# Optimization experiments

Hardware: AMD Instinct MI355X
Metric: run time of the kernel (lower is better)

Reference implementation:

```python
import jax, jax.numpy as jnp
import numpy as np

EPS_BN = 1e-5
EPS_NORM = 1e-12


def setup_inputs() -> dict:
    dim, mid, k = 128, 32, 3
    b, h, w = 8, 128, 128
    key = jax.random.key(0)
    ks = jax.random.split(key, 16)
    s = 0.05
    return {
        "x": jax.random.normal(ks[0], (b, dim, h, w), jnp.float32),
        "w_spatial_in": jax.random.normal(ks[1], (dim, dim), jnp.float32) * s,
        "w_dw_spatial": jax.random.normal(ks[2], (dim, 1, k), jnp.float32) * s,
        "w_spatial_out": jax.random.normal(ks[3], (dim, dim), jnp.float32) * s,
        "w_ch_in": jax.random.normal(ks[4], (dim, dim), jnp.float32) * s,
        "w_ch_dw": jax.random.normal(ks[5], (dim, 1, k), jnp.float32) * s,
        "w_ch_out": jax.random.normal(ks[6], (dim, dim), jnp.float32) * s,
        "w_mlp1": jax.random.normal(ks[7], (mid, dim), jnp.float32) * s,
        "b_mlp1": jax.random.normal(ks[8], (mid,), jnp.float32) * s,
        "w_mlp2": jax.random.normal(ks[9], (dim, mid), jnp.float32) * s,
        "b_mlp2": jax.random.normal(ks[10], (dim,), jnp.float32) * s,
        "diff_weight": jnp.float32(1.0),
        "bn_gamma": jnp.ones((dim,), jnp.float32),
        "bn_beta": jnp.zeros((dim,), jnp.float32),
        "w_out_proj": jax.random.normal(ks[11], (dim, dim), jnp.float32) * s,
    }


def _dwconv1d(seq, wk):
    # seq: [b, c, L], wk: [c, 1, k] depthwise, 'same' padding
    c = seq.shape[1]
    k = wk.shape[-1]
    return jax.lax.conv_general_dilated(
        seq, wk, window_strides=(1,), padding=[(k // 2, k // 2)],
        dimension_numbers=("NCH", "OIH", "NCH"), feature_group_count=c)


def _ocs_forward(x, w_spatial_in, w_dw_spatial, w_spatial_out,
                 w_ch_in, w_ch_dw, w_ch_out,
                 w_mlp1, b_mlp1, w_mlp2, b_mlp2,
                 diff_weight, bn_gamma, bn_beta, w_out_proj):
    b, c, h, w = x.shape
    L = h * w
    alpha = beta = eta = 1.0

    # ---- scan indices (4 orders) ----
    idx_row = jnp.arange(L)
    gy, gx = jnp.meshgrid(jnp.arange(h), jnp.arange(w), indexing="ij")
    idx_col = (gx * h + gy).reshape(-1)
    orders = [idx_row, idx_row[::-1], idx_col, idx_col[::-1]]

    x_seq0 = x.reshape(b, c, L).transpose(0, 2, 1)  # [b, L, c]

    def scan(idx):
        s = x_seq0[:, idx]                                   # gather   [b,L,c]
        s = jnp.einsum("blc,oc->blo", s, w_spatial_in)       # linear
        s = _dwconv1d(s.transpose(0, 2, 1), w_dw_spatial)    # dw conv  [b,c,L]
        s = jnp.einsum("bcl,oc->blo", s, w_spatial_out)      # linear   [b,L,c]
        s = s.at[:, idx].set(s[:, jnp.arange(L)]) if False else s[:, jnp.argsort(idx)]  # scatter back (inverse perm)
        return s.transpose(0, 2, 1).reshape(b, c, h, w)

    y_sp = (scan(orders[0]) + scan(orders[1]) + scan(orders[2]) + scan(orders[3])) * 0.25

    # ---- channel branch ----
    seq = x.reshape(b, c, L)
    seq = jnp.einsum("oc,bcl->bol", w_ch_in, seq)
    seq = _dwconv1d(seq, w_ch_dw)
    seq = jnp.einsum("oc,bcl->bol", w_ch_out, seq)
    gap = x.mean((2, 3))                                     # [b,c]
    gap = gap / jnp.maximum(jnp.linalg.norm(gap, axis=1, keepdims=True), EPS_NORM)
    m = jnp.einsum("bi,bj->bij", gap, gap)                   # [b,c,c]
    seq_agg = jnp.einsum("bij,bjl->bil", m, seq)             # [b,c,L]
    h1 = jax.nn.silu(jnp.einsum("mc,bcl->bml", w_mlp1, seq_agg) + b_mlp1[None, :, None])
    y_ch = (jnp.einsum("cm,bml->bcl", w_mlp2, h1) + b_mlp2[None, :, None]).reshape(b, c, h, w)

    # ---- difference branch (reflect-pad 4-neighbor abs diff) ----
    p = jnp.pad(x, ((0, 0), (0, 0), (1, 1), (1, 1)), mode="reflect")
    cx = p[:, :, 1:-1, 1:-1]
    diff = (jnp.abs(cx - p[:, :, 1:-1, :-2]) + jnp.abs(cx - p[:, :, 1:-1, 2:])
            + jnp.abs(cx - p[:, :, :-2, 1:-1]) + jnp.abs(cx - p[:, :, 2:, 1:-1])) * 0.25
    y_diff = x + diff_weight * diff

    # ---- combine, 1x1 proj, batchnorm (training-mode batch stats) ----
    y = alpha * y_sp + beta * y_ch + eta * y_diff
    y = jnp.einsum("oc,bchw->bohw", w_out_proj, y)
    mu = y.mean((0, 2, 3))
    var = y.var((0, 2, 3))
    y = (y - mu[None, :, None, None]) * jax.lax.rsqrt(var + EPS_BN)[None, :, None, None]
    y = y * bn_gamma[None, :, None, None] + bn_beta[None, :, None, None]
    return y


def reference(x, w_spatial_in, w_dw_spatial, w_spatial_out, w_ch_in, w_ch_dw,
              w_ch_out, w_mlp1, b_mlp1, w_mlp2, b_mlp2, diff_weight,
              bn_gamma, bn_beta, w_out_proj):
    return _ocs_forward(x, w_spatial_in, w_dw_spatial, w_spatial_out,
                        w_ch_in, w_ch_dw, w_ch_out, w_mlp1, b_mlp1,
                        w_mlp2, b_mlp2, diff_weight, bn_gamma, bn_beta,
                        w_out_proj)
```

## Files before the change

### kernel.cpp

```cpp
#include <hip/hip_runtime.h>
#include <hip/hip_bf16.h>

#define C 128
#define L 16384
#define B 8
#define MID 32
#define NBL (B * L)

typedef unsigned short ushort_t;
typedef __attribute__((ext_vector_type(8))) short s8v;
typedef __attribute__((ext_vector_type(4))) float f4v;
typedef __attribute__((ext_vector_type(8))) float f8v;

__device__ __forceinline__ unsigned short f2bf(float f) {
    union { float f; unsigned int u; } a; a.f = f;
    unsigned int u = a.u;
    return (unsigned short)((u + 0x7fffu + ((u >> 16) & 1u)) >> 16);
}

__device__ __forceinline__ f8v unp8(s8v v) {
    f8v f;
#pragma unroll
    for (int j = 0; j < 8; j++) f[j] = __uint_as_float(((unsigned int)(unsigned short)v[j]) << 16);
    return f;
}

__device__ __forceinline__ f8v ldf8(const float* p) {
    float4 a = *(const float4*)p;
    float4 b = *(const float4*)(p + 4);
    f8v f;
    f[0] = a.x; f[1] = a.y; f[2] = a.z; f[3] = a.w;
    f[4] = b.x; f[5] = b.y; f[6] = b.z; f[7] = b.w;
    return f;
}

__device__ __forceinline__ int widx(int slot, int o, int w) {
    return ((slot * 8 + (o >> 4)) * 64 + (w >> 3) * 16 + (o & 15)) * 8 + (w & 7);
}

__global__ __launch_bounds__(256) void k_cvt(const float* __restrict__ x,
                                             ushort_t* __restrict__ xb,
                                             float* __restrict__ gap) {
    __shared__ float xs[64][129];
    const int bid = blockIdx.x;
    const int b = bid >> 8;
    const int l0 = (bid & 255) * 64;
    const int tid = threadIdx.x;
    const int c = tid >> 1, h = tid & 1;
    const float* src = x + ((size_t)(b * C + c)) * L + l0 + h * 32;
    float s = 0.f;
#pragma unroll
    for (int j = 0; j < 8; j++) {
        float4 v = *(const float4*)(src + j * 4);
        s += (v.x + v.y) + (v.z + v.w);
        int lb = h * 32 + j * 4;
        xs[lb + 0][c] = v.x; xs[lb + 1][c] = v.y;
        xs[lb + 2][c] = v.z; xs[lb + 3][c] = v.w;
    }
    s += __shfl_xor(s, 1);
    if (h == 0) atomicAdd(&gap[b * C + c], s);
    __syncthreads();
    const int l = tid & 63, quarter = tid >> 6, cb = quarter * 32;
    union { ushort_t hh[32]; uint4 q[4]; } u;
#pragma unroll
    for (int k = 0; k < 32; k++) u.hh[k] = f2bf(xs[l][cb + k]);
    uint4* dst = (uint4*)(xb + ((size_t)(b * L + l0 + l)) * C + cb);
#pragma unroll
    for (int k = 0; k < 4; k++) dst[k] = u.q[k];
}

__global__ __launch_bounds__(128) void k_prep(const float* __restrict__ Win,
                                              const float* __restrict__ Wproj,
                                              const float* __restrict__ Wout,
                                              const float* __restrict__ w2,
                                              const float* __restrict__ b2,
                                              const float* __restrict__ wds,
                                              const float* __restrict__ gap,
                                              const float* __restrict__ w1,
                                              const float* __restrict__ Wco,
                                              const float* __restrict__ wcd,
                                              const float* __restrict__ Wci,
                                              ushort_t* __restrict__ Wf,
                                              float* __restrict__ bp,
                                              float* __restrict__ a,
                                              float* __restrict__ pv) {
    const int bid = blockIdx.x;
    const int c = threadIdx.x;
    if (bid < 128) {
        const int o = bid;
        __shared__ float pr[C];
        __shared__ float wct[C];
        pr[c] = Wproj[o * C + c];
        __syncthreads();
        {
            float s = 0.f;
            for (int k = 0; k < C; k++) s = fmaf(pr[k], Wout[k * C + c], s);
            wct[c] = s;
        }
        __syncthreads();
        float a1 = 0.f, as = 0.f;
        for (int cc = 0; cc < C; cc++) {
            float w = wct[cc];
            float win = Win[cc * C + c];
            a1 = fmaf(w * wds[3 * cc + 1], win, a1);
            as = fmaf(w * (0.25f * (wds[3 * cc] + wds[3 * cc + 2])), win, as);
        }
        const int slot = c >> 5, wi = c & 31;
        Wf[widx(slot, o, wi)] = f2bf(a1);
        Wf[widx(4 + slot, o, wi)] = f2bf(as);
        Wf[widx(8 + slot, o, wi)] = f2bf(pr[c]);
        if (c < MID) {
            float s2 = 0.f;
            for (int k = 0; k < C; k++) s2 = fmaf(pr[k], w2[k * MID + c], s2);
            Wf[widx(12, o, c)] = f2bf(s2);
        }
        if (c == 0) {
            float s3 = 0.f;
            for (int k = 0; k < C; k++) s3 = fmaf(pr[k], b2[k], s3);
            bp[o] = s3;
        }
    } else {
        const int b = bid - 128;
        __shared__ float gl[C];
        __shared__ float red[C];
        __shared__ float gws[C];
        float v = gap[b * C + c] * (1.f / (float)L);
        red[c] = v * v;
        __syncthreads();
        for (int w = 64; w > 0; w >>= 1) {
            if (c < w) red[c] += red[c + w];
            __syncthreads();
        }
        float nrm = fmaxf(sqrtf(red[0]), 1e-12f);
        gl[c] = v / nrm;
        __syncthreads();
        if (c < MID) {
            float s = 0.f;
            for (int k = 0; k < C; k++) s = fmaf(w1[c * C + k], gl[k], s);
            a[b * MID + c] = s;
        }
        {
            float s = 0.f;
            for (int k = 0; k < C; k++) s = fmaf(gl[k], Wco[k * C + c], s);
            gws[c] = s;
        }
        __syncthreads();
        float p0 = 0.f, p1 = 0.f, p2 = 0.f;
        for (int cc = 0; cc < C; cc++) {
            float wv = Wci[cc * C + c];
            float g = gws[cc];
            p0 = fmaf(g * wcd[3 * cc], wv, p0);
            p1 = fmaf(g * wcd[3 * cc + 1], wv, p1);
            p2 = fmaf(g * wcd[3 * cc + 2], wv, p2);
        }
        pv[b * 384 + c] = p0;
        pv[b * 384 + 128 + c] = p1;
        pv[b * 384 + 256 + c] = p2;
    }
}

__global__ __launch_bounds__(1024) __attribute__((amdgpu_waves_per_eu(4, 4)))
void k_fused(const ushort_t* __restrict__ xb,
             const ushort_t* __restrict__ Wf,
             const float* __restrict__ pv,
             const float* __restrict__ a,
             const float* __restrict__ b1,
             const float* __restrict__ pdw,
             const float* __restrict__ bp,
             float* __restrict__ outp,
             float* __restrict__ stats) {
    __shared__ ushort_t wlf[53248];
    __shared__ float spv[384];
    __shared__ float sdst[C];
    __shared__ float sdsq[C];
    const int tid = threadIdx.x;
    const int bid = blockIdx.x;
    const int b = bid & 7;
    const int rg = bid >> 3;

#pragma unroll
    for (int i = 0; i < 7; i++) {
        int idx = tid + i * 1024;
        if (idx < 6656) ((uint4*)wlf)[idx] = ((const uint4*)Wf)[idx];
    }
    if (tid < 384) spv[tid] = pv[b * 384 + tid];
    if (tid < C) { sdst[tid] = 0.f; sdsq[tid] = 0.f; }

    const int wave = tid >> 6, lane = tid & 63;
    const int n = lane & 15, q = lane >> 4;
    const int xg = (wave & 7) * 16 + n;
    const float dwt4 = pdw[0] * 0.25f;
    const size_t rb = (size_t)b * L;

    __syncthreads();

#define AF(slot, mt) (*(const s8v*)(wlf + ((((slot) * 8 + (mt)) * 64 + lane) * 8)))

#pragma unroll 1
    for (int iter = 0; iter < 2; iter++) {
        const int y = rg * 4 + iter * 2 + (wave >> 3);
        const int l = y * 128 + xg;

        const int rL = (l > 0) ? (l - 1) : -1;
        const int rR = (l < L - 1) ? (l + 1) : -1;
        const int rU = (y > 0) ? (l - 128) : ((xg > 0) ? (16256 + xg - 1) : -1);
        const int rD = (y < 127) ? (l + 128) : ((xg < 127) ? (xg + 1) : -1);
        const ushort_t* xrow = xb + (rb + l) * C;
        const ushort_t* prL = xb + (rb + ((rL >= 0) ? rL : 0)) * C;
        const ushort_t* prR = xb + (rb + ((rR >= 0) ? rR : 0)) * C;
        const ushort_t* prU = xb + (rb + ((rU >= 0) ? rU : 0)) * C;
        const ushort_t* prD = xb + (rb + ((rD >= 0) ? rD : 0)) * C;

        float s1 = 0.f;
#pragma unroll
        for (int ks = 0; ks < 4; ks++) {
            const int c0 = ks * 32 + q * 8;
            {
                f8v xv = unp8(*(const s8v*)(xrow + c0));
                f8v p = ldf8(spv + 128 + c0);
#pragma unroll
                for (int j = 0; j < 8; j++) s1 = fmaf(p[j], xv[j], s1);
            }
            {
                f8v xv = unp8(*(const s8v*)(prL + c0));
                if (rL < 0) {
#pragma unroll
                    for (int j = 0; j < 8; j++) xv[j] = 0.f;
                }
                f8v p = ldf8(spv + c0);
#pragma unroll
                for (int j = 0; j < 8; j++) s1 = fmaf(p[j], xv[j], s1);
            }
            {
                f8v xv = unp8(*(const s8v*)(prR + c0));
                if (rR < 0) {
#pragma unroll
                    for (int j = 0; j < 8; j++) xv[j] = 0.f;
                }
                f8v p = ldf8(spv + 256 + c0);
#pragma unroll
                for (int j = 0; j < 8; j++) s1 = fmaf(p[j], xv[j], s1);
            }
        }
        s1 += __shfl_xor(s1, 16);
        s1 += __shfl_xor(s1, 32);

        f4v acc[8];
#pragma unroll
        for (int i = 0; i < 8; i++) acc[i] = (f4v){0.f, 0.f, 0.f, 0.f};

        {
            f8v av = ldf8(a + b * MID + q * 8);
            f8v bv = ldf8(b1 + q * 8);
            s8v fs;
#pragma unroll
            for (int j = 0; j < 8; j++) {
                float pre = fmaf(av[j], s1, bv[j]);
                fs[j] = (short)f2bf(pre / (1.f + __expf(-pre)));
            }
#pragma unroll
            for (int mt = 0; mt < 8; mt++)
                acc[mt] = __builtin_amdgcn_mfma_f32_16x16x32_bf16(AF(12, mt), fs, acc[mt], 0, 0, 0);
        }

#pragma unroll
        for (int ks = 0; ks < 4; ks++) {
            const int c0 = ks * 32 + q * 8;
            s8v vc = *(const s8v*)(xrow + c0);
            s8v vl = *(const s8v*)(prL + c0);
            s8v vr = *(const s8v*)(prR + c0);
            s8v vu = *(const s8v*)(prU + c0);
            s8v vd = *(const s8v*)(prD + c0);
            if (rL < 0) vl = (s8v){0, 0, 0, 0, 0, 0, 0, 0};
            if (rR < 0) vr = (s8v){0, 0, 0, 0, 0, 0, 0, 0};
            if (rU < 0) vu = (s8v){0, 0, 0, 0, 0, 0, 0, 0};
            if (rD < 0) vd = (s8v){0, 0, 0, 0, 0, 0, 0, 0};

#pragma unroll
            for (int mt = 0; mt < 8; mt++)
                acc[mt] = __builtin_amdgcn_mfma_f32_16x16x32_bf16(AF(ks, mt), vc, acc[mt], 0, 0, 0);
#pragma unroll
            for (int mt = 0; mt < 8; mt++) {
                s8v af = AF(4 + ks, mt);
                acc[mt] = __builtin_amdgcn_mfma_f32_16x16x32_bf16(af, vl, acc[mt], 0, 0, 0);
                acc[mt] = __builtin_amdgcn_mfma_f32_16x16x32_bf16(af, vr, acc[mt], 0, 0, 0);
                acc[mt] = __builtin_amdgcn_mfma_f32_16x16x32_bf16(af, vu, acc[mt], 0, 0, 0);
                acc[mt] = __builtin_amdgcn_mfma_f32_16x16x32_bf16(af, vd, acc[mt], 0, 0, 0);
            }

            f8v xc = unp8(vc);
            f8v d8;
            {
                f8v t = unp8((xg > 0) ? vl : vr);
#pragma unroll
                for (int j = 0; j < 8; j++) d8[j] = fabsf(xc[j] - t[j]);
            }
            {
                f8v t = unp8((xg < 127) ? vr : vl);
#pragma unroll
                for (int j = 0; j < 8; j++) d8[j] += fabsf(xc[j] - t[j]);
            }
            {
                f8v t = unp8((y > 0) ? vu : vd);
#pragma unroll
                for (int j = 0; j < 8; j++) d8[j] += fabsf(xc[j] - t[j]);
            }
            {
                f8v t = unp8((y < 127) ? vd : vu);
#pragma unroll
                for (int j = 0; j < 8; j++) d8[j] += fabsf(xc[j] - t[j]);
            }
            s8v vy;
#pragma unroll
            for (int j = 0; j < 8; j++) vy[j] = (short)f2bf(fmaf(dwt4, d8[j], xc[j]));
#pragma unroll
            for (int mt = 0; mt < 8; mt++)
                acc[mt] = __builtin_amdgcn_mfma_f32_16x16x32_bf16(AF(8 + ks, mt), vy, acc[mt], 0, 0, 0);
        }

#pragma unroll
        for (int mt = 0; mt < 8; mt++) {
            const int o0 = mt * 16 + q * 4;
            float4 bv4 = *(const float4*)(bp + o0);
#pragma unroll
            for (int i = 0; i < 4; i++) {
                float bai = (i == 0) ? bv4.x : (i == 1) ? bv4.y : (i == 2) ? bv4.z : bv4.w;
                float v = acc[mt][i] + bai;
                outp[((size_t)(b * C + o0 + i)) * L + l] = v;
                float s = v, sq = v * v;
                s += __shfl_xor(s, 1); sq += __shfl_xor(sq, 1);
                s += __shfl_xor(s, 2); sq += __shfl_xor(sq, 2);
                s += __shfl_xor(s, 4); sq += __shfl_xor(sq, 4);
                s += __shfl_xor(s, 8); sq += __shfl_xor(sq, 8);
                if (n == 0) {
                    atomicAdd(&sdst[o0 + i], s);
                    atomicAdd(&sdsq[o0 + i], sq);
                }
            }
        }
    }

#undef AF

    __syncthreads();
    if (tid < C) {
        atomicAdd(&stats[tid], sdst[tid]);
        atomicAdd(&stats[C + tid], sdsq[tid]);
    }
}

__global__ __launch_bounds__(256) void k_bnapply(float* __restrict__ outp,
                                                 const float* __restrict__ stats,
                                                 const float* __restrict__ gamma,
                                                 const float* __restrict__ beta) {
    int bo = blockIdx.x;
    int o = bo & (C - 1);
    float nn = (float)NBL;
    float mu = stats[o] / nn;
    float var = stats[C + o] / nn - mu * mu;
    float sc = gamma[o] * rsqrtf(var + 1e-5f);
    float sh = fmaf(-mu, sc, beta[o]);
    float4* p = (float4*)(outp + (size_t)bo * L);
    for (int i = threadIdx.x; i < L / 4; i += 256) {
        float4 v = p[i];
        v.x = fmaf(v.x, sc, sh);
        v.y = fmaf(v.y, sc, sh);
        v.z = fmaf(v.z, sc, sh);
        v.w = fmaf(v.w, sc, sh);
        p[i] = v;
    }
}

extern "C" void kernel_launch(void* const* d_in, const int* in_sizes, int n_in,
                              void* d_out, int out_size, void* d_ws, size_t ws_size,
                              hipStream_t stream) {
    const float* x = (const float*)d_in[0];
    const float* Win = (const float*)d_in[1];
    const float* wds = (const float*)d_in[2];
    const float* Wout = (const float*)d_in[3];
    const float* Wci = (const float*)d_in[4];
    const float* wcd = (const float*)d_in[5];
    const float* Wco = (const float*)d_in[6];
    const float* w1 = (const float*)d_in[7];
    const float* b1 = (const float*)d_in[8];
    const float* w2 = (const float*)d_in[9];
    const float* b2 = (const float*)d_in[10];
    const float* pdw = (const float*)d_in[11];
    const float* gamma = (const float*)d_in[12];
    const float* beta = (const float*)d_in[13];
    const float* Wproj = (const float*)d_in[14];

    char* wsb = (char*)d_ws;
    ushort_t* xb = (ushort_t*)wsb;
    ushort_t* Wf = (ushort_t*)(wsb + 33554432);
    char* S = wsb + 176160768;
    float* gap  = (float*)(S + 0);
    float* stats= (float*)(S + 4096);
    float* a    = (float*)(S + 6144);
    float* bp   = (float*)(S + 8192);
    float* pv   = (float*)(S + 12288);
    float* outp = (float*)d_out;

    hipMemsetAsync(S, 0, 5120, stream);
    k_cvt<<<2048, 256, 0, stream>>>(x, xb, gap);
    k_prep<<<136, 128, 0, stream>>>(Win, Wproj, Wout, w2, b2, wds,
                                    gap, w1, Wco, wcd, Wci, Wf, bp, a, pv);
    k_fused<<<256, 1024, 0, stream>>>(xb, Wf, pv, a, b1, pdw, bp, outp, stats);
    k_bnapply<<<1024, 256, 0, stream>>>(outp, stats, gamma, beta);
}
```

Baseline: 279.2 us.

## Sum neighbor inputs before MFMA, split output channels across wave pairs

The four neighbor rows share one weight slot, so the main kernel now adds them in fp32 and packs the sum to bf16 for a single MFMA per tile. This removes three quarters of the neighbor MFMAs. Each wave now computes half of the output channels (4 m-tiles) over 4 rows instead of 8 m-tiles over 2 rows, which halves the accumulator registers but makes each input row load twice. The cvt kernel also changes its global load pattern to contiguous float4 rows per channel and computes the channel sums from shared memory. Rounding the neighbor sum to bf16 before the MFMA changes the numerics slightly.

```diff
diff --git a/kernel.cpp b/kernel.cpp
--- a/kernel.cpp
+++ b/kernel.cpp
@@ -23,6 +23,13 @@
 #pragma unroll
     for (int j = 0; j < 8; j++) f[j] = __uint_as_float(((unsigned int)(unsigned short)v[j]) << 16);
     return f;
+}
+
+__device__ __forceinline__ s8v pk8(f8v f) {
+    s8v v;
+#pragma unroll
+    for (int j = 0; j < 8; j++) v[j] = (short)f2bf(f[j]);
+    return v;
 }
 
 __device__ __forceinline__ f8v ldf8(const float* p) {
@@ -46,27 +53,31 @@
     const int b = bid >> 8;
     const int l0 = (bid & 255) * 64;
     const int tid = threadIdx.x;
-    const int c = tid >> 1, h = tid & 1;
-    const float* src = x + ((size_t)(b * C + c)) * L + l0 + h * 32;
-    float s = 0.f;
-#pragma unroll
-    for (int j = 0; j < 8; j++) {
-        float4 v = *(const float4*)(src + j * 4);
-        s += (v.x + v.y) + (v.z + v.w);
-        int lb = h * 32 + j * 4;
-        xs[lb + 0][c] = v.x; xs[lb + 1][c] = v.y;
-        xs[lb + 2][c] = v.z; xs[lb + 3][c] = v.w;
-    }
-    s += __shfl_xor(s, 1);
-    if (h == 0) atomicAdd(&gap[b * C + c], s);
+    const int rr = tid >> 4;
+    const int col = (tid & 15) * 4;
+#pragma unroll
+    for (int pass = 0; pass < 8; pass++) {
+        const int c = pass * 16 + rr;
+        float4 v = *(const float4*)(x + ((size_t)(b * C + c)) * L + l0 + col);
+        xs[col + 0][c] = v.x; xs[col + 1][c] = v.y;
+        xs[col + 2][c] = v.z; xs[col + 3][c] = v.w;
+    }
     __syncthreads();
+    {
+        const int c = tid >> 1, h = tid & 1;
+        float s = 0.f;
+#pragma unroll
+        for (int k = 0; k < 32; k++) s += xs[h * 32 + k][c];
+        s += __shfl_xor(s, 1);
+        if (h == 0) atomicAdd(&gap[b * C + c], s);
+    }
     const int l = tid & 63, quarter = tid >> 6, cb = quarter * 32;
-    union { ushort_t hh[32]; uint4 q[4]; } u;
+    union { ushort_t hh[32]; uint4 qv[4]; } u;
 #pragma unroll
     for (int k = 0; k < 32; k++) u.hh[k] = f2bf(xs[l][cb + k]);
     uint4* dst = (uint4*)(xb + ((size_t)(b * L + l0 + l)) * C + cb);
 #pragma unroll
-    for (int k = 0; k < 4; k++) dst[k] = u.q[k];
+    for (int k = 0; k < 4; k++) dst[k] = u.qv[k];
 }
 
 __global__ __launch_bounds__(128) void k_prep(const float* __restrict__ Win,
@@ -187,18 +198,20 @@
     if (tid < C) { sdst[tid] = 0.f; sdsq[tid] = 0.f; }
 
     const int wave = tid >> 6, lane = tid & 63;
+    const int half = wave & 1;
+    const int lg = wave >> 1;
     const int n = lane & 15, q = lane >> 4;
-    const int xg = (wave & 7) * 16 + n;
+    const int xg = lg * 16 + n;
     const float dwt4 = pdw[0] * 0.25f;
     const size_t rb = (size_t)b * L;
 
     __syncthreads();
 
-#define AF(slot, mt) (*(const s8v*)(wlf + ((((slot) * 8 + (mt)) * 64 + lane) * 8)))
+#define AF(slot, mt) (*(const s8v*)(wlf + ((((slot) * 8 + (half * 4 + mt)) * 64 + lane) * 8)))
 
 #pragma unroll 1
-    for (int iter = 0; iter < 2; iter++) {
-        const int y = rg * 4 + iter * 2 + (wave >> 3);
+    for (int iter = 0; iter < 4; iter++) {
+        const int y = rg * 4 + iter;
         const int l = y * 128 + xg;
 
         const int rL = (l > 0) ? (l - 1) : -1;
@@ -245,9 +258,9 @@
         s1 += __shfl_xor(s1, 16);
         s1 += __shfl_xor(s1, 32);
 
-        f4v acc[8];
-#pragma unroll
-        for (int i = 0; i < 8; i++) acc[i] = (f4v){0.f, 0.f, 0.f, 0.f};
+        f4v acc[4];
+#pragma unroll
+        for (int i = 0; i < 4; i++) acc[i] = (f4v){0.f, 0.f, 0.f, 0.f};
 
         {
             f8v av = ldf8(a + b * MID + q * 8);
@@ -259,7 +272,7 @@
                 fs[j] = (short)f2bf(pre / (1.f + __expf(-pre)));
             }
 #pragma unroll
-            for (int mt = 0; mt < 8; mt++)
+            for (int mt = 0; mt < 4; mt++)
                 acc[mt] = __builtin_amdgcn_mfma_f32_16x16x32_bf16(AF(12, mt), fs, acc[mt], 0, 0, 0);
         }
 
@@ -267,60 +280,71 @@
         for (int ks = 0; ks < 4; ks++) {
             const int c0 = ks * 32 + q * 8;
             s8v vc = *(const s8v*)(xrow + c0);
-            s8v vl = *(const s8v*)(prL + c0);
-            s8v vr = *(const s8v*)(prR + c0);
-            s8v vu = *(const s8v*)(prU + c0);
-            s8v vd = *(const s8v*)(prD + c0);
-            if (rL < 0) vl = (s8v){0, 0, 0, 0, 0, 0, 0, 0};
-            if (rR < 0) vr = (s8v){0, 0, 0, 0, 0, 0, 0, 0};
-            if (rU < 0) vu = (s8v){0, 0, 0, 0, 0, 0, 0, 0};
-            if (rD < 0) vd = (s8v){0, 0, 0, 0, 0, 0, 0, 0};
-
-#pragma unroll
-            for (int mt = 0; mt < 8; mt++)
+#pragma unroll
+            for (int mt = 0; mt < 4; mt++)
                 acc[mt] = __builtin_amdgcn_mfma_f32_16x16x32_bf16(AF(ks, mt), vc, acc[mt], 0, 0, 0);
-#pragma unroll
-            for (int mt = 0; mt < 8; mt++) {
-                s8v af = AF(4 + ks, mt);
-                acc[mt] = __builtin_amdgcn_mfma_f32_16x16x32_bf16(af, vl, acc[mt], 0, 0, 0);
-                acc[mt] = __builtin_amdgcn_mfma_f32_16x16x32_bf16(af, vr, acc[mt], 0, 0, 0);
-                acc[mt] = __builtin_amdgcn_mfma_f32_16x16x32_bf16(af, vu, acc[mt], 0, 0, 0);
-                acc[mt] = __builtin_amdgcn_mfma_f32_16x16x32_bf16(af, vd, acc[mt], 0, 0, 0);
-            }
-
             f8v xc = unp8(vc);
-            f8v d8;
-            {
-                f8v t = unp8((xg > 0) ? vl : vr);
-#pragma unroll
-                for (int j = 0; j < 8; j++) d8[j] = fabsf(xc[j] - t[j]);
-            }
-            {
-                f8v t = unp8((xg < 127) ? vr : vl);
-#pragma unroll
-                for (int j = 0; j < 8; j++) d8[j] += fabsf(xc[j] - t[j]);
-            }
-            {
-                f8v t = unp8((y > 0) ? vu : vd);
-#pragma unroll
-                for (int j = 0; j < 8; j++) d8[j] += fabsf(xc[j] - t[j]);
-            }
-            {
-                f8v t = unp8((y < 127) ? vd : vu);
-#pragma unroll
-                for (int j = 0; j < 8; j++) d8[j] += fabsf(xc[j] - t[j]);
-            }
-            s8v vy;
-#pragma unroll
-            for (int j = 0; j < 8; j++) vy[j] = (short)f2bf(fmaf(dwt4, d8[j], xc[j]));
-#pragma unroll
-            for (int mt = 0; mt < 8; mt++)
-                acc[mt] = __builtin_amdgcn_mfma_f32_16x16x32_bf16(AF(8 + ks, mt), vy, acc[mt], 0, 0, 0);
-        }
-
-#pragma unroll
-        for (int mt = 0; mt < 8; mt++) {
-            const int o0 = mt * 16 + q * 4;
+
+            f8v sum, d8;
+            {
+                s8v vl = *(const s8v*)(prL + c0);
+                s8v vr = *(const s8v*)(prR + c0);
+                f8v xl = unp8(vl);
+                f8v xr = unp8(vr);
+                if (rL < 0) {
+#pragma unroll
+                    for (int j = 0; j < 8; j++) xl[j] = 0.f;
+                }
+                if (rR < 0) {
+#pragma unroll
+                    for (int j = 0; j < 8; j++) xr[j] = 0.f;
+                }
+                sum = xl + xr;
+                f8v a1 = (xg > 0) ? xl : xr;
+                f8v a2 = (xg < 127) ? xr : xl;
+#pragma unroll
+                for (int j = 0; j < 8; j++)
+                    d8[j] = fabsf(xc[j] - a1[j]) + fabsf(xc[j] - a2[j]);
+            }
+            {
+                s8v vu = *(const s8v*)(prU + c0);
+                s8v vd = *(const s8v*)(prD + c0);
+                f8v xu = unp8(vu);
+                f8v xd = unp8(vd);
+                if (rU < 0) {
+#pragma unroll
+                    for (int j = 0; j < 8; j++) xu[j] = 0.f;
+                }
+                if (rD < 0) {
+#pragma unroll
+                    for (int j = 0; j < 8; j++) xd[j] = 0.f;
+                }
+                sum = sum + (xu + xd);
+                f8v a3 = (y > 0) ? xu : xd;
+                f8v a4 = (y < 127) ? xd : xu;
+#pragma unroll
+                for (int j = 0; j < 8; j++)
+                    d8[j] += fabsf(xc[j] - a3[j]) + fabsf(xc[j] - a4[j]);
+            }
+            {
+                s8v vs = pk8(sum);
+#pragma unroll
+                for (int mt = 0; mt < 4; mt++)
+                    acc[mt] = __builtin_amdgcn_mfma_f32_16x16x32_bf16(AF(4 + ks, mt), vs, acc[mt], 0, 0, 0);
+            }
+            {
+                s8v vy;
+#pragma unroll
+                for (int j = 0; j < 8; j++) vy[j] = (short)f2bf(fmaf(dwt4, d8[j], xc[j]));
+#pragma unroll
+                for (int mt = 0; mt < 4; mt++)
+                    acc[mt] = __builtin_amdgcn_mfma_f32_16x16x32_bf16(AF(8 + ks, mt), vy, acc[mt], 0, 0, 0);
+            }
+        }
+
+#pragma unroll
+        for (int mt = 0; mt < 4; mt++) {
+            const int o0 = (half * 4 + mt) * 16 + q * 4;
             float4 bv4 = *(const float4*)(bp + o0);
 #pragma unroll
             for (int i = 0; i < 4; i++) {
```

Result: slower. 731.7 us (+162.1%).
